# Performance work log

Hardware: AMD Instinct MI355X
Metric: run time of the kernel (lower is better)

The kernel has to match this reference:

```python
import jax, jax.numpy as jnp
import numpy as np

D_MODEL = 1024
NUM_HEADS = 16
D_K = D_MODEL // NUM_HEADS


def setup_inputs() -> dict:
    key = jax.random.key(0)
    ks = jax.random.split(key, 9)
    s = 1.0 / np.sqrt(D_MODEL)
    inp = {
        'x': jax.random.normal(ks[0], (1, 4096, D_MODEL), dtype=jnp.float32),
        'W_q': jax.random.uniform(ks[1], (D_MODEL, D_MODEL), jnp.float32, -s, s),
        'b_q': jax.random.uniform(ks[2], (D_MODEL,), jnp.float32, -s, s),
        'W_k': jax.random.uniform(ks[3], (D_MODEL, D_MODEL), jnp.float32, -s, s),
        'b_k': jax.random.uniform(ks[4], (D_MODEL,), jnp.float32, -s, s),
        'W_v': jax.random.uniform(ks[5], (D_MODEL, D_MODEL), jnp.float32, -s, s),
        'b_v': jax.random.uniform(ks[6], (D_MODEL,), jnp.float32, -s, s),
        'W_o': jax.random.uniform(ks[7], (D_MODEL, D_MODEL), jnp.float32, -s, s),
        'b_o': jax.random.uniform(ks[8], (D_MODEL,), jnp.float32, -s, s),
    }
    return inp


def reference(x, W_q, b_q, W_k, b_k, W_v, b_v, W_o, b_o):
    B, S, _ = x.shape
    def split_heads(t):  # [B,S,D] -> [B,H,S,d_k]
        return t.reshape(B, S, NUM_HEADS, D_K).transpose(0, 2, 1, 3)
    Q = split_heads(x @ W_q + b_q)
    K = split_heads(x @ W_k + b_k)
    V = split_heads(x @ W_v + b_v)
    scale = 1.0 / jnp.sqrt(jnp.float32(D_K))
    scores = jnp.einsum('bhqd,bhkd->bhqk', Q, K) * scale  # [B,H,S,S]
    attn = jax.nn.softmax(scores, axis=-1)
    ctx = jnp.einsum('bhqk,bhkd->bhqd', attn, V)
    ctx = ctx.transpose(0, 2, 1, 3).reshape(B, S, D_MODEL)
    return ctx @ W_o + b_o
```

## Files before the change

kernel.cpp:

```cpp
#include <hip/hip_runtime.h>
#include <hip/hip_bf16.h>
#include <stdint.h>


#define DM 1024
#define SEQ 4096
#define NH 16
#define DK 64

#define QSCALE 0.18033688011112042f

typedef __attribute__((ext_vector_type(8))) short bf16x8;
typedef __attribute__((ext_vector_type(4))) float f32x4;
typedef __attribute__((ext_vector_type(2))) uint32_t u32x2;

__device__ __forceinline__ short f2bf(float f) {
  union { float f; uint32_t u; } x; x.f = f;
  uint32_t r = x.u + 0x7fffu + ((x.u >> 16) & 1u);
  return (short)(r >> 16);
}

__device__ __forceinline__ void gl_lds16(const void* g, void* l) {
  __builtin_amdgcn_global_load_lds(
      (const __attribute__((address_space(1))) void*)g,
      (__attribute__((address_space(3))) void*)l, 16, 0, 0);
}

__global__ __launch_bounds__(256) void cvt_x_k(const float* __restrict__ in,
                                               short* __restrict__ out) {
  size_t i = (size_t)blockIdx.x * 256 + threadIdx.x;
  const float4* ip = (const float4*)in;
  float4 a = ip[2 * i], b = ip[2 * i + 1];
  bf16x8 o;
  o[0] = f2bf(a.x); o[1] = f2bf(a.y); o[2] = f2bf(a.z); o[3] = f2bf(a.w);
  o[4] = f2bf(b.x); o[5] = f2bf(b.y); o[6] = f2bf(b.z); o[7] = f2bf(b.w);
  *(bf16x8*)(out + 8 * i) = o;
}

__global__ __launch_bounds__(256) void cvt_wt_k(const float* __restrict__ W0,
                                                const float* __restrict__ W1,
                                                const float* __restrict__ W2,
                                                const float* __restrict__ W3,
                                                short* __restrict__ Wt0) {
  __shared__ alignas(16) short T[64][66];
  const int z = blockIdx.z;
  const float* W = (z == 0) ? W0 : (z == 1) ? W1 : (z == 2) ? W2 : W3;
  short* Wt = Wt0 + (size_t)z * (DM * DM);
  const int k0 = blockIdx.y * 64, n0 = blockIdx.x * 64;
#pragma unroll
  for (int rep = 0; rep < 16; ++rep) {
    int lin = rep * 256 + threadIdx.x;
    int i = lin >> 6, j = lin & 63;
    T[i][j] = f2bf(W[(size_t)(k0 + i) * DM + n0 + j]);
  }
  __syncthreads();
#pragma unroll
  for (int rep = 0; rep < 16; ++rep) {
    int lin = rep * 256 + threadIdx.x;
    int n = lin >> 6, kk = lin & 63;
    Wt[(size_t)(n0 + n) * DM + k0 + kk] = T[kk][n];
  }
}

__global__ __launch_bounds__(256) void trans_v_k(const short* __restrict__ V,
                                                 short* __restrict__ Vt) {
  __shared__ alignas(16) short T[64][66];
  const int s0 = blockIdx.x * 64, h = blockIdx.y;
#pragma unroll
  for (int rep = 0; rep < 16; ++rep) {
    int lin = rep * 256 + threadIdx.x;
    int i = lin >> 6, j = lin & 63;
    T[i][j] = V[(size_t)(s0 + i) * DM + h * DK + j];
  }
  __syncthreads();
#pragma unroll
  for (int rep = 0; rep < 16; ++rep) {
    int lin = rep * 256 + threadIdx.x;
    int d = lin >> 6, ss = lin & 63;
    int sp = ((ss & 15) << 2) + (ss >> 4);
    Vt[((size_t)h * DK + d) * SEQ + s0 + sp] = T[ss][d];
  }
}

__global__ __launch_bounds__(256) void gemm_qkv(
    const short* __restrict__ xb, const short* __restrict__ Wt0,
    const float* __restrict__ bq, const float* __restrict__ bk,
    const float* __restrict__ bv, short* __restrict__ out0) {
  const int z = blockIdx.z;
  const short* Bt = Wt0 + (size_t)z * (DM * DM);
  const float* bias = (z == 0) ? bq : (z == 1) ? bk : bv;
  const float qs = (z == 0) ? QSCALE : 1.0f;
  short* out = out0 + (size_t)z * ((size_t)SEQ * DM);

  __shared__ alignas(16) short As[128 * 32];
  __shared__ alignas(16) short Bs[128 * 32];
  const int tid = threadIdx.x, lane = tid & 63, w = tid >> 6;
  const int bm = blockIdx.y * 128, bn = blockIdx.x * 128;
  const int wm = (w >> 1) * 64, wn = (w & 1) * 64;
  f32x4 acc[4][4] = {};

  for (int kt = 0; kt < DM; kt += 32) {
    __syncthreads();
#pragma unroll
    for (int c = 0; c < 2; ++c) {
      int i = w * 2 + c;
      int ob = i * 1024 + lane * 16;
      int row = ob >> 6, colb = ob & 63;
      gl_lds16((const char*)xb + ((size_t)(bm + row) * DM + kt) * 2 + colb,
               (char*)As + i * 1024);
      gl_lds16((const char*)Bt + ((size_t)(bn + row) * DM + kt) * 2 + colb,
               (char*)Bs + i * 1024);
    }
    __syncthreads();
    bf16x8 bfr[4];
#pragma unroll
    for (int n = 0; n < 4; ++n)
      bfr[n] = *(const bf16x8*)((const char*)Bs +
                                (wn + n * 16 + (lane & 15)) * 64 + (lane >> 4) * 16);
#pragma unroll
    for (int m = 0; m < 4; ++m) {
      bf16x8 af = *(const bf16x8*)((const char*)As +
                                   (wm + m * 16 + (lane & 15)) * 64 + (lane >> 4) * 16);
#pragma unroll
      for (int n = 0; n < 4; ++n)
        acc[m][n] = __builtin_amdgcn_mfma_f32_16x16x32_bf16(af, bfr[n], acc[m][n], 0, 0, 0);
    }
  }
  const int r0 = bm + wm + ((lane >> 4) << 2);
  const int c0 = bn + wn + (lane & 15);
#pragma unroll
  for (int n = 0; n < 4; ++n) {
    const int col = c0 + n * 16;
    const float b = bias[col];
#pragma unroll
    for (int m = 0; m < 4; ++m)
#pragma unroll
      for (int r = 0; r < 4; ++r)
        out[(size_t)(r0 + m * 16 + r) * DM + col] = f2bf((acc[m][n][r] + b) * qs);
  }
}

__global__ __launch_bounds__(256) void gemm_out(
    const short* __restrict__ A, const short* __restrict__ Bt,
    const float* __restrict__ bias, float* __restrict__ out) {
  __shared__ alignas(16) short As[128 * 32];
  __shared__ alignas(16) short Bs[128 * 32];
  const int tid = threadIdx.x, lane = tid & 63, w = tid >> 6;
  const int bm = blockIdx.y * 128, bn = blockIdx.x * 128;
  const int wm = (w >> 1) * 64, wn = (w & 1) * 64;
  f32x4 acc[4][4] = {};

  for (int kt = 0; kt < DM; kt += 32) {
    __syncthreads();
#pragma unroll
    for (int c = 0; c < 2; ++c) {
      int i = w * 2 + c;
      int ob = i * 1024 + lane * 16;
      int row = ob >> 6, colb = ob & 63;
      gl_lds16((const char*)A + ((size_t)(bm + row) * DM + kt) * 2 + colb,
               (char*)As + i * 1024);
      gl_lds16((const char*)Bt + ((size_t)(bn + row) * DM + kt) * 2 + colb,
               (char*)Bs + i * 1024);
    }
    __syncthreads();
    bf16x8 bfr[4];
#pragma unroll
    for (int n = 0; n < 4; ++n)
      bfr[n] = *(const bf16x8*)((const char*)Bs +
                                (wn + n * 16 + (lane & 15)) * 64 + (lane >> 4) * 16);
#pragma unroll
    for (int m = 0; m < 4; ++m) {
      bf16x8 af = *(const bf16x8*)((const char*)As +
                                   (wm + m * 16 + (lane & 15)) * 64 + (lane >> 4) * 16);
#pragma unroll
      for (int n = 0; n < 4; ++n)
        acc[m][n] = __builtin_amdgcn_mfma_f32_16x16x32_bf16(af, bfr[n], acc[m][n], 0, 0, 0);
    }
  }
  const int r0 = bm + wm + ((lane >> 4) << 2);
  const int c0 = bn + wn + (lane & 15);
#pragma unroll
  for (int n = 0; n < 4; ++n) {
    const int col = c0 + n * 16;
    const float b = bias[col];
#pragma unroll
    for (int m = 0; m < 4; ++m)
#pragma unroll
      for (int r = 0; r < 4; ++r)
        out[(size_t)(r0 + m * 16 + r) * DM + col] = acc[m][n][r] + b;
  }
}

__global__ __launch_bounds__(256) void attn_k(
    const short* __restrict__ Qb, const short* __restrict__ Kb,
    const short* __restrict__ Vt, short* __restrict__ ctx) {
  const int h = blockIdx.y, qt = blockIdx.x;
  const int tid = threadIdx.x, lane = tid & 63, w = tid >> 6;
  __shared__ alignas(16) short Ks[2][64 * 64];
  __shared__ alignas(16) short Vs[2][64 * 64];
  __shared__ alignas(16) short Pl[4][16 * 64];

  const int qr = qt * 64 + w * 16 + (lane & 15);
  const short* qp = Qb + (size_t)qr * DM + h * DK + ((lane >> 4) * 8);
  const bf16x8 qf0 = *(const bf16x8*)qp;
  const bf16x8 qf1 = *(const bf16x8*)(qp + 32);

  bf16x8 ones;
#pragma unroll
  for (int j = 0; j < 8; ++j) ones[j] = (short)0x3F80;

  f32x4 o[4] = {};
  f32x4 ol = {};
  float m = -3000.f;

  const int xk = (lane & 7) << 4;
  char* pbase = (char*)&Pl[w][0];
  const int g = lane >> 4, cl = lane & 15;

  auto stage = [&](int buf, int s0) {
#pragma unroll
    for (int c = 0; c < 2; ++c) {
      int i = w * 2 + c;
      int ob = i * 1024 + lane * 16;
      int row = ob >> 7, colb = ob & 127;
      int src = colb ^ ((row & 7) << 4);
      gl_lds16((const char*)Kb + ((size_t)(s0 + row) * DM + h * DK) * 2 + src,
               (char*)&Ks[buf][0] + i * 1024);
      gl_lds16((const char*)Vt + ((size_t)(h * DK + row) * SEQ + s0) * 2 + src,
               (char*)&Vs[buf][0] + i * 1024);
    }
  };

  stage(0, 0);

  for (int t = 0; t < SEQ / 64; ++t) {
    const int cur = t & 1;
    __syncthreads();
    if (t < SEQ / 64 - 1) stage(cur ^ 1, (t + 1) * 64);

    const char* kbase = (const char*)&Ks[cur][0];
    const char* vbase = (const char*)&Vs[cur][0];

    f32x4 sc[4] = {};
    __builtin_amdgcn_s_setprio(1);
#pragma unroll
    for (int kk = 0; kk < 2; ++kk) {
      bf16x8 a = kk ? qf1 : qf0;
#pragma unroll
      for (int n = 0; n < 4; ++n) {
        bf16x8 b = *(const bf16x8*)(kbase + (n * 16 + cl) * 128 +
                                    ((kk * 64 + g * 16) ^ xk));
        sc[n] = __builtin_amdgcn_mfma_f32_16x16x32_bf16(a, b, sc[n], 0, 0, 0);
      }
    }
    __builtin_amdgcn_s_setprio(0);

    float lm = fmaxf(fmaxf(fmaxf(sc[0][0], sc[0][1]), fmaxf(sc[0][2], sc[0][3])),
                     fmaxf(fmaxf(sc[1][0], sc[1][1]), fmaxf(sc[1][2], sc[1][3])));
    lm = fmaxf(lm, fmaxf(fmaxf(fmaxf(sc[2][0], sc[2][1]), fmaxf(sc[2][2], sc[2][3])),
                         fmaxf(fmaxf(sc[3][0], sc[3][1]), fmaxf(sc[3][2], sc[3][3]))));
    lm = fmaxf(lm, __shfl_xor(lm, 1));
    lm = fmaxf(lm, __shfl_xor(lm, 2));
    lm = fmaxf(lm, __shfl_xor(lm, 4));
    lm = fmaxf(lm, __shfl_xor(lm, 8));
    if (!__all(lm <= m + 8.f)) {
      float mn = fmaxf(m, lm);
      float al = exp2f(m - mn);
      m = mn;
#pragma unroll
      for (int n = 0; n < 4; ++n) {
        o[n][0] *= al; o[n][1] *= al; o[n][2] *= al; o[n][3] *= al;
      }
      ol[0] *= al; ol[1] *= al; ol[2] *= al; ol[3] *= al;
    }

#pragma unroll
    for (int r = 0; r < 4; ++r) {
      const int prow = g * 4 + r;
      float p0 = exp2f(sc[0][r] - m), p1 = exp2f(sc[1][r] - m);
      float p2 = exp2f(sc[2][r] - m), p3 = exp2f(sc[3][r] - m);
      uint32_t u0, u1;
      asm("v_cvt_pk_bf16_f32 %0, %1, %2" : "=v"(u0) : "v"(p0), "v"(p1));
      asm("v_cvt_pk_bf16_f32 %0, %1, %2" : "=v"(u1) : "v"(p2), "v"(p3));
      u32x2 uu; uu[0] = u0; uu[1] = u1;
      *(u32x2*)(pbase + prow * 128 + ((cl * 8) ^ ((prow & 7) << 4))) = uu;
    }

    __builtin_amdgcn_s_setprio(1);
#pragma unroll
    for (int kk = 0; kk < 2; ++kk) {
      bf16x8 pa = *(const bf16x8*)(pbase + cl * 128 + ((kk * 64 + g * 16) ^ xk));
      ol = __builtin_amdgcn_mfma_f32_16x16x32_bf16(pa, ones, ol, 0, 0, 0);
#pragma unroll
      for (int n = 0; n < 4; ++n) {
        bf16x8 vb = *(const bf16x8*)(vbase + (n * 16 + cl) * 128 +
                                     ((kk * 64 + g * 16) ^ xk));
        o[n] = __builtin_amdgcn_mfma_f32_16x16x32_bf16(pa, vb, o[n], 0, 0, 0);
      }
    }
    __builtin_amdgcn_s_setprio(0);
  }

#pragma unroll
  for (int r = 0; r < 4; ++r) {
    float inv = 1.f / ol[r];
    int row = qt * 64 + w * 16 + g * 4 + r;
#pragma unroll
    for (int n = 0; n < 4; ++n)
      ctx[(size_t)row * DM + h * DK + n * 16 + cl] = f2bf(o[n][r] * inv);
  }
}

extern "C" void kernel_launch(void* const* d_in, const int* in_sizes, int n_in,
                              void* d_out, int out_size, void* d_ws, size_t ws_size,
                              hipStream_t stream) {
  const float* x  = (const float*)d_in[0];
  const float* Wq = (const float*)d_in[1];
  const float* bq = (const float*)d_in[2];
  const float* Wk = (const float*)d_in[3];
  const float* bk = (const float*)d_in[4];
  const float* Wv = (const float*)d_in[5];
  const float* bv = (const float*)d_in[6];
  const float* Wo = (const float*)d_in[7];
  const float* bo = (const float*)d_in[8];

  char* ws = (char*)d_ws;
  short* xb  = (short*)(ws + (size_t)0);
  short* Wt  = (short*)(ws + ((size_t)8 << 20));
  short* Qb  = (short*)(ws + ((size_t)16 << 20));
  short* Kb  = (short*)(ws + ((size_t)24 << 20));
  short* Vb  = (short*)(ws + ((size_t)32 << 20));
  short* Vt  = (short*)(ws + ((size_t)40 << 20));
  short* ctx = (short*)(ws + ((size_t)48 << 20));

  cvt_x_k<<<2048, 256, 0, stream>>>(x, xb);
  cvt_wt_k<<<dim3(16, 16, 4), 256, 0, stream>>>(Wq, Wk, Wv, Wo, Wt);
  gemm_qkv<<<dim3(DM / 128, SEQ / 128, 3), 256, 0, stream>>>(xb, Wt, bq, bk, bv, Qb);
  trans_v_k<<<dim3(SEQ / 64, NH), 256, 0, stream>>>(Vb, Vt);
  attn_k<<<dim3(SEQ / 64, NH), 256, 0, stream>>>(Qb, Kb, Vt, ctx);
  gemm_out<<<dim3(DM / 128, SEQ / 128), 256, 0, stream>>>(
      ctx, Wt + (size_t)3 * (DM * DM), bo, (float*)d_out);
}
```

Measured before the change: 291.4 us.

## Double-buffer GEMM staging, fold running max into MFMA accumulator, use DPP reductions

Both projection GEMMs now use two LDS buffers, so the next K tile is fetched while the current one is multiplied, with MFMA priority raised during compute. The attention kernel seeds the score MFMA accumulator with the negated running max, which removes the per-element subtraction before exp2, and replaces the shuffle-based row max with DPP row operations. This doubles LDS use in the GEMMs, and the max-folding changes how the rescale logic tracks the offset.

```diff
diff --git a/kernel.cpp b/kernel.cpp
--- a/kernel.cpp
+++ b/kernel.cpp
@@ -24,6 +24,14 @@
   __builtin_amdgcn_global_load_lds(
       (const __attribute__((address_space(1))) void*)g,
       (__attribute__((address_space(3))) void*)l, 16, 0, 0);
+}
+
+template <int CTRL>
+__device__ __forceinline__ float dppmax(float x) {
+  union { float f; int i; } u; u.f = x;
+  int p = __builtin_amdgcn_update_dpp(u.i, u.i, CTRL, 0xf, 0xf, false);
+  union { int i; float f; } v; v.i = p;
+  return fmaxf(x, v.f);
 }
 
 __global__ __launch_bounds__(256) void cvt_x_k(const float* __restrict__ in,
@@ -92,39 +100,46 @@
   const float qs = (z == 0) ? QSCALE : 1.0f;
   short* out = out0 + (size_t)z * ((size_t)SEQ * DM);
 
-  __shared__ alignas(16) short As[128 * 32];
-  __shared__ alignas(16) short Bs[128 * 32];
+  __shared__ alignas(16) short As[2][128 * 32];
+  __shared__ alignas(16) short Bs[2][128 * 32];
   const int tid = threadIdx.x, lane = tid & 63, w = tid >> 6;
   const int bm = blockIdx.y * 128, bn = blockIdx.x * 128;
   const int wm = (w >> 1) * 64, wn = (w & 1) * 64;
   f32x4 acc[4][4] = {};
 
-  for (int kt = 0; kt < DM; kt += 32) {
-    __syncthreads();
+  auto stage = [&](int buf, int kt) {
 #pragma unroll
     for (int c = 0; c < 2; ++c) {
       int i = w * 2 + c;
       int ob = i * 1024 + lane * 16;
       int row = ob >> 6, colb = ob & 63;
       gl_lds16((const char*)xb + ((size_t)(bm + row) * DM + kt) * 2 + colb,
-               (char*)As + i * 1024);
+               (char*)&As[buf][0] + i * 1024);
       gl_lds16((const char*)Bt + ((size_t)(bn + row) * DM + kt) * 2 + colb,
-               (char*)Bs + i * 1024);
-    }
+               (char*)&Bs[buf][0] + i * 1024);
+    }
+  };
+
+  stage(0, 0);
+  for (int t = 0; t < DM / 32; ++t) {
+    const int cur = t & 1;
     __syncthreads();
+    if (t < DM / 32 - 1) stage(cur ^ 1, (t + 1) * 32);
     bf16x8 bfr[4];
 #pragma unroll
     for (int n = 0; n < 4; ++n)
-      bfr[n] = *(const bf16x8*)((const char*)Bs +
+      bfr[n] = *(const bf16x8*)((const char*)&Bs[cur][0] +
                                 (wn + n * 16 + (lane & 15)) * 64 + (lane >> 4) * 16);
+    __builtin_amdgcn_s_setprio(1);
 #pragma unroll
     for (int m = 0; m < 4; ++m) {
-      bf16x8 af = *(const bf16x8*)((const char*)As +
+      bf16x8 af = *(const bf16x8*)((const char*)&As[cur][0] +
                                    (wm + m * 16 + (lane & 15)) * 64 + (lane >> 4) * 16);
 #pragma unroll
       for (int n = 0; n < 4; ++n)
         acc[m][n] = __builtin_amdgcn_mfma_f32_16x16x32_bf16(af, bfr[n], acc[m][n], 0, 0, 0);
     }
+    __builtin_amdgcn_s_setprio(0);
   }
   const int r0 = bm + wm + ((lane >> 4) << 2);
   const int c0 = bn + wn + (lane & 15);
@@ -143,39 +158,46 @@
 __global__ __launch_bounds__(256) void gemm_out(
     const short* __restrict__ A, const short* __restrict__ Bt,
     const float* __restrict__ bias, float* __restrict__ out) {
-  __shared__ alignas(16) short As[128 * 32];
-  __shared__ alignas(16) short Bs[128 * 32];
+  __shared__ alignas(16) short As[2][128 * 32];
+  __shared__ alignas(16) short Bs[2][128 * 32];
   const int tid = threadIdx.x, lane = tid & 63, w = tid >> 6;
   const int bm = blockIdx.y * 128, bn = blockIdx.x * 128;
   const int wm = (w >> 1) * 64, wn = (w & 1) * 64;
   f32x4 acc[4][4] = {};
 
-  for (int kt = 0; kt < DM; kt += 32) {
-    __syncthreads();
+  auto stage = [&](int buf, int kt) {
 #pragma unroll
     for (int c = 0; c < 2; ++c) {
       int i = w * 2 + c;
       int ob = i * 1024 + lane * 16;
       int row = ob >> 6, colb = ob & 63;
       gl_lds16((const char*)A + ((size_t)(bm + row) * DM + kt) * 2 + colb,
-               (char*)As + i * 1024);
+               (char*)&As[buf][0] + i * 1024);
       gl_lds16((const char*)Bt + ((size_t)(bn + row) * DM + kt) * 2 + colb,
-               (char*)Bs + i * 1024);
-    }
+               (char*)&Bs[buf][0] + i * 1024);
+    }
+  };
+
+  stage(0, 0);
+  for (int t = 0; t < DM / 32; ++t) {
+    const int cur = t & 1;
     __syncthreads();
+    if (t < DM / 32 - 1) stage(cur ^ 1, (t + 1) * 32);
     bf16x8 bfr[4];
 #pragma unroll
     for (int n = 0; n < 4; ++n)
-      bfr[n] = *(const bf16x8*)((const char*)Bs +
+      bfr[n] = *(const bf16x8*)((const char*)&Bs[cur][0] +
                                 (wn + n * 16 + (lane & 15)) * 64 + (lane >> 4) * 16);
+    __builtin_amdgcn_s_setprio(1);
 #pragma unroll
     for (int m = 0; m < 4; ++m) {
-      bf16x8 af = *(const bf16x8*)((const char*)As +
+      bf16x8 af = *(const bf16x8*)((const char*)&As[cur][0] +
                                    (wm + m * 16 + (lane & 15)) * 64 + (lane >> 4) * 16);
 #pragma unroll
       for (int n = 0; n < 4; ++n)
         acc[m][n] = __builtin_amdgcn_mfma_f32_16x16x32_bf16(af, bfr[n], acc[m][n], 0, 0, 0);
     }
+    __builtin_amdgcn_s_setprio(0);
   }
   const int r0 = bm + wm + ((lane >> 4) << 2);
   const int c0 = bn + wn + (lane & 15);
@@ -211,7 +233,7 @@
 
   f32x4 o[4] = {};
   f32x4 ol = {};
-  float m = -3000.f;
+  f32x4 mvec = {3000.f, 3000.f, 3000.f, 3000.f};
 
   const int xk = (lane & 7) << 4;
   char* pbase = (char*)&Pl[w][0];
@@ -241,17 +263,14 @@
     const char* kbase = (const char*)&Ks[cur][0];
     const char* vbase = (const char*)&Vs[cur][0];
 
-    f32x4 sc[4] = {};
+    f32x4 sc[4];
     __builtin_amdgcn_s_setprio(1);
 #pragma unroll
-    for (int kk = 0; kk < 2; ++kk) {
-      bf16x8 a = kk ? qf1 : qf0;
-#pragma unroll
-      for (int n = 0; n < 4; ++n) {
-        bf16x8 b = *(const bf16x8*)(kbase + (n * 16 + cl) * 128 +
-                                    ((kk * 64 + g * 16) ^ xk));
-        sc[n] = __builtin_amdgcn_mfma_f32_16x16x32_bf16(a, b, sc[n], 0, 0, 0);
-      }
+    for (int n = 0; n < 4; ++n) {
+      bf16x8 b0 = *(const bf16x8*)(kbase + (n * 16 + cl) * 128 + ((g * 16) ^ xk));
+      sc[n] = __builtin_amdgcn_mfma_f32_16x16x32_bf16(qf0, b0, mvec, 0, 0, 0);
+      bf16x8 b1 = *(const bf16x8*)(kbase + (n * 16 + cl) * 128 + ((64 + g * 16) ^ xk));
+      sc[n] = __builtin_amdgcn_mfma_f32_16x16x32_bf16(qf1, b1, sc[n], 0, 0, 0);
     }
     __builtin_amdgcn_s_setprio(0);
 
@@ -259,26 +278,27 @@
                      fmaxf(fmaxf(sc[1][0], sc[1][1]), fmaxf(sc[1][2], sc[1][3])));
     lm = fmaxf(lm, fmaxf(fmaxf(fmaxf(sc[2][0], sc[2][1]), fmaxf(sc[2][2], sc[2][3])),
                          fmaxf(fmaxf(sc[3][0], sc[3][1]), fmaxf(sc[3][2], sc[3][3]))));
-    lm = fmaxf(lm, __shfl_xor(lm, 1));
-    lm = fmaxf(lm, __shfl_xor(lm, 2));
-    lm = fmaxf(lm, __shfl_xor(lm, 4));
-    lm = fmaxf(lm, __shfl_xor(lm, 8));
-    if (!__all(lm <= m + 8.f)) {
-      float mn = fmaxf(m, lm);
-      float al = exp2f(m - mn);
-      m = mn;
+    lm = dppmax<0xB1>(lm);
+    lm = dppmax<0x4E>(lm);
+    lm = dppmax<0x141>(lm);
+    lm = dppmax<0x140>(lm);
+    if (!__all(lm <= 8.f)) {
+      float dm = fmaxf(lm, 0.f);
+      float al = exp2f(-dm);
 #pragma unroll
       for (int n = 0; n < 4; ++n) {
         o[n][0] *= al; o[n][1] *= al; o[n][2] *= al; o[n][3] *= al;
+        sc[n][0] -= dm; sc[n][1] -= dm; sc[n][2] -= dm; sc[n][3] -= dm;
       }
       ol[0] *= al; ol[1] *= al; ol[2] *= al; ol[3] *= al;
+      mvec[0] -= dm; mvec[1] -= dm; mvec[2] -= dm; mvec[3] -= dm;
     }
 
 #pragma unroll
     for (int r = 0; r < 4; ++r) {
       const int prow = g * 4 + r;
-      float p0 = exp2f(sc[0][r] - m), p1 = exp2f(sc[1][r] - m);
-      float p2 = exp2f(sc[2][r] - m), p3 = exp2f(sc[3][r] - m);
+      float p0 = exp2f(sc[0][r]), p1 = exp2f(sc[1][r]);
+      float p2 = exp2f(sc[2][r]), p3 = exp2f(sc[3][r]);
       uint32_t u0, u1;
       asm("v_cvt_pk_bf16_f32 %0, %1, %2" : "=v"(u0) : "v"(p0), "v"(p1));
       asm("v_cvt_pk_bf16_f32 %0, %1, %2" : "=v"(u1) : "v"(p2), "v"(p3));
```

Result: slower. 298.7 us (+2.5%).
